# Optimization experiments

Hardware: AMD Instinct MI355X
Metric: run time of the kernel (lower is better)

The kernel has to match this reference:

```python
import jax, jax.numpy as jnp
import numpy as np

N = 50000        # nodes
E = 800000       # edges (before self-loops)
F_IN = 128       # input_features
HID = 160        # hidden_sf(5) * model_dim(32)
OUT_C = 128      # out_sf(4) * output_channels(32)
NGR = 64         # number of graphs in batch
OUT_DIM = 10
K = 5            # hops per SGConv


def setup_inputs() -> dict:
    key = jax.random.key(0)
    ks = jax.random.split(key, 12)
    x = jax.random.normal(ks[0], (N, F_IN), dtype=jnp.float32)
    edge_index = jax.random.randint(ks[1], (2, E), 0, N, dtype=jnp.int64)
    batch = jnp.sort(jax.random.randint(ks[2], (N,), 0, NGR, dtype=jnp.int64))
    s = 0.05
    W1 = jax.random.normal(ks[3], (F_IN, HID), dtype=jnp.float32) * s
    b1 = jnp.zeros((HID,), dtype=jnp.float32)
    W2 = jax.random.normal(ks[4], (HID, HID), dtype=jnp.float32) * s
    b2 = jnp.zeros((HID,), dtype=jnp.float32)
    W3 = jax.random.normal(ks[5], (HID, OUT_C), dtype=jnp.float32) * s
    b3 = jnp.zeros((OUT_C,), dtype=jnp.float32)
    fc_w = jax.random.normal(ks[6], (OUT_C, OUT_DIM), dtype=jnp.float32) * s
    fc_b = jnp.zeros((OUT_DIM,), dtype=jnp.float32)
    return {"x": x, "edge_index": edge_index, "batch": batch,
            "W1": W1, "b1": b1, "W2": W2, "b2": b2, "W3": W3, "b3": b3,
            "fc_w": fc_w, "fc_b": fc_b}


def reference(x, edge_index, batch, W1, b1, W2, b2, W3, b3, fc_w, fc_b):
    # gcn_norm: add self-loops, symmetric normalization D^-1/2 A D^-1/2
    loop = jnp.arange(N, dtype=edge_index.dtype)
    src = jnp.concatenate([edge_index[0], loop])   # [E+N]
    dst = jnp.concatenate([edge_index[1], loop])
    deg = jax.ops.segment_sum(jnp.ones(E + N, dtype=x.dtype), dst, num_segments=N)
    dinv = jnp.where(deg > 0, deg ** -0.5, 0.0)
    norm = (dinv[src] * dinv[dst])[:, None]        # [E+N, 1]

    def prop(h):
        # one hop of normalized propagation: gather at src, scatter-add at dst
        return jax.ops.segment_sum(h[src] * norm, dst, num_segments=N)

    def sgconv(h, W, b):
        for _ in range(K):
            h = prop(h)
        return h @ W + b

    h = sgconv(x, W1, b1)
    h = sgconv(h, W2, b2)
    h = sgconv(h, W3, b3)

    # global_mean_pool over batch indices
    counts = jax.ops.segment_sum(jnp.ones(N, dtype=h.dtype), batch, num_segments=NGR)
    pooled = jax.ops.segment_sum(h, batch, num_segments=NGR)
    pooled = pooled / jnp.maximum(counts, 1.0)[:, None]

    logits = pooled @ fc_w + fc_b
    return jax.nn.log_softmax(logits, axis=1)
```

## Files before the change

### kernel.cpp

```cpp
#include <hip/hip_runtime.h>

constexpr int N    = 50000;
constexpr int E    = 800000;
constexpr int NG   = 64;
constexpr int ODIM = 10;
constexpr int OUTC = 128;
constexpr int GP_BLOCKS = 256;
constexpr int SCAN_B = (N + 255) / 256;
constexpr int CS1B   = 784;
constexpr float SCALE    = 32768.0f;
constexpr float INVSCALE = 1.0f / SCALE;

constexpr int CNT_C = 16;
constexpr int CHUNK = E / CNT_C;
constexpr int CNT_R = 8;
constexpr int RANGE = N / CNT_R;
constexpr int NV4   = CHUNK / 4;
constexpr int HV4   = NV4 / 2;

typedef float floatx2 __attribute__((ext_vector_type(2)));

__device__ __forceinline__ void unp4(unsigned int u, float* f) {
    floatx2 lo = __builtin_amdgcn_cvt_pk_f32_fp8(u, false);
    floatx2 hi = __builtin_amdgcn_cvt_pk_f32_fp8(u, true);
    f[0] = lo.x; f[1] = lo.y; f[2] = hi.x; f[3] = hi.y;
}
__device__ __forceinline__ unsigned int pk4(float a, float b, float c, float d) {
    int r = __builtin_amdgcn_cvt_pk_fp8_f32(a, b, 0, false);
    r = __builtin_amdgcn_cvt_pk_fp8_f32(c, d, r, true);
    return (unsigned int)r;
}

__global__ void k_init_small(int* cntg, float* svec) {
    int i = threadIdx.x;
    if (i < NG) cntg[i] = 0;
    if (i < 128) svec[i] = 0.f;
}

__device__ __forceinline__ void cnt4_src(int4 v, int lo, int* h,
                                         int* __restrict__ pos_e, int e) {
    if ((unsigned)(v.x - lo) < (unsigned)RANGE) pos_e[e]     = atomicAdd(&h[v.x - lo], 1);
    if ((unsigned)(v.y - lo) < (unsigned)RANGE) pos_e[e + 1] = atomicAdd(&h[v.y - lo], 1);
    if ((unsigned)(v.z - lo) < (unsigned)RANGE) pos_e[e + 2] = atomicAdd(&h[v.z - lo], 1);
    if ((unsigned)(v.w - lo) < (unsigned)RANGE) pos_e[e + 3] = atomicAdd(&h[v.w - lo], 1);
}
__device__ __forceinline__ void cnt4_dst(int4 v, int lo, int* h) {
    if ((unsigned)(v.x - lo) < (unsigned)RANGE) atomicAdd(&h[v.x - lo], 1);
    if ((unsigned)(v.y - lo) < (unsigned)RANGE) atomicAdd(&h[v.y - lo], 1);
    if ((unsigned)(v.z - lo) < (unsigned)RANGE) atomicAdd(&h[v.z - lo], 1);
    if ((unsigned)(v.w - lo) < (unsigned)RANGE) atomicAdd(&h[v.w - lo], 1);
}

__global__ __launch_bounds__(512) void k_count(const int* __restrict__ ei,
        int* __restrict__ cnt16, int* __restrict__ deg16, int* __restrict__ pos_e) {
    __shared__ int h[RANGE];
    int bid  = blockIdx.x;
    int c    = bid & 15;
    int r    = (bid >> 4) & 7;
    int kind = bid >> 7;
    int tid  = threadIdx.x;
    for (int i = tid; i < RANGE; i += 512) h[i] = 0;
    __syncthreads();
    int lo = r * RANGE;
    const int4* src = (const int4*)(ei + (size_t)kind * E + (size_t)c * CHUNK);
    int ebase = c * CHUNK;
    if (kind == 0) {
        for (int i = tid; i < HV4; i += 512) {
            int4 a = src[i];
            int4 b = src[i + HV4];
            cnt4_src(a, lo, h, pos_e, ebase + i * 4);
            cnt4_src(b, lo, h, pos_e, ebase + (i + HV4) * 4);
        }
    } else {
        for (int i = tid; i < HV4; i += 512) {
            int4 a = src[i];
            int4 b = src[i + HV4];
            cnt4_dst(a, lo, h);
            cnt4_dst(b, lo, h);
        }
    }
    __syncthreads();
    int* dst = (kind == 0 ? cnt16 : deg16) + (size_t)c * N + lo;
    for (int i = tid; i < RANGE; i += 512) dst[i] = h[i];
}

__global__ void k_scan1(const int* __restrict__ cnt16, int* __restrict__ base16,
                        int* __restrict__ off, int* bsum,
                        const int* __restrict__ deg16, float* wsq, float* sdeg) {
    __shared__ int buf[256];
    int tid = threadIdx.x;
    int i = blockIdx.x * 256 + tid;
    int total = 0;
    if (i < N) {
        int run = 0;
        #pragma unroll
        for (int q = 0; q < CNT_C; ++q) {
            base16[q * N + i] = run;
            run += cnt16[q * N + i];
        }
        total = run;
        int deg = 1;
        #pragma unroll
        for (int q = 0; q < CNT_C; ++q) deg += deg16[q * N + i];
        float d = (float)deg;
        wsq[i]  = 1.0f / d;
        sdeg[i] = sqrtf(d);
    }
    buf[tid] = total;
    __syncthreads();
    for (int s = 1; s < 256; s <<= 1) {
        int add = (tid >= s) ? buf[tid - s] : 0;
        __syncthreads();
        buf[tid] += add;
        __syncthreads();
    }
    if (i < N) off[i] = buf[tid] - total;
    if (tid == 255) bsum[blockIdx.x] = buf[255];
}

__global__ void k_scan2(int* bsum, int* off) {
    __shared__ int buf[256];
    int tid = threadIdx.x;
    int v = (tid < SCAN_B) ? bsum[tid] : 0;
    buf[tid] = v;
    __syncthreads();
    for (int s = 1; s < 256; s <<= 1) {
        int add = (tid >= s) ? buf[tid - s] : 0;
        __syncthreads();
        buf[tid] += add;
        __syncthreads();
    }
    if (tid < SCAN_B) bsum[tid] = buf[tid] - v;
    if (tid == 0) off[N] = E;
}

__global__ void k_scan3(int* off, const int* __restrict__ bsum) {
    int i = blockIdx.x * 256 + threadIdx.x;
    if (i < N) off[i] += bsum[blockIdx.x];
}

__global__ void k_cntg(const int* __restrict__ batch, int* cntg) {
    __shared__ int h[NG];
    if (threadIdx.x < NG) h[threadIdx.x] = 0;
    __syncthreads();
    int i = blockIdx.x * 256 + threadIdx.x;
    if (i < N) atomicAdd(&h[batch[i]], 1);
    __syncthreads();
    if (threadIdx.x < NG && h[threadIdx.x]) atomicAdd(&cntg[threadIdx.x], h[threadIdx.x]);
}

__global__ void k_fill(const int* __restrict__ ei, const int* __restrict__ off,
                       const int* __restrict__ base16, const int* __restrict__ pos_e,
                       int* __restrict__ mdst,
                       const int* __restrict__ batch, const int* __restrict__ cntg,
                       const float* __restrict__ sdeg, uint4* Z0) {
    int e = blockIdx.x * 256 + threadIdx.x;
    if (e < E) {
        int s = ei[e];
        int q = e / CHUNK;
        mdst[off[s] + base16[q * N + s] + pos_e[e]] = ei[E + e];
    }
    if (e < N) {
        int i = e;
        int g = batch[i];
        int c = cntg[g]; if (c < 1) c = 1;
        float v = (SCALE / (float)c) / sdeg[i];
        unsigned int byte = (unsigned int)(__builtin_amdgcn_cvt_pk_fp8_f32(v, v, 0, false) & 0xFF);
        uint4 rows[4];
        #pragma unroll
        for (int q = 0; q < 4; ++q) rows[q] = make_uint4(0u, 0u, 0u, 0u);
        unsigned int* wp = (unsigned int*)rows;
        wp[g >> 2] = byte << (8 * (g & 3));
        #pragma unroll
        for (int q = 0; q < 4; ++q) Z0[(size_t)i * 4 + q] = rows[q];
    }
}

__device__ __forceinline__ void add16(float* acc, uint4 g) {
    float f[16];
    unp4(g.x, f); unp4(g.y, f + 4); unp4(g.z, f + 8); unp4(g.w, f + 12);
    #pragma unroll
    for (int k = 0; k < 16; ++k) acc[k] += f[k];
}

__global__ __launch_bounds__(256) void k_prop(
        const uint4* __restrict__ zin, uint2* __restrict__ zout,
        const int* __restrict__ off, const int* __restrict__ mdst,
        const float* __restrict__ wsq) {
    int t = blockIdx.x * 256 + threadIdx.x;
    int node = t >> 3;
    int sub  = (t >> 2) & 1;
    int c    = t & 3;
    if (node >= N) return;

    float acc[16];
    #pragma unroll
    for (int k = 0; k < 16; ++k) acc[k] = 0.f;

    int a = off[node], b = off[node + 1];
    int half = (b - a + 1) >> 1;
    int e  = sub ? a + half : a;
    int e1 = sub ? b : a + half;
    if (!sub) {
        add16(acc, zin[(size_t)node * 4 + c]);
    }
    for (; e + 7 < e1; e += 8) {
        int d0 = mdst[e],     d1 = mdst[e + 1], d2 = mdst[e + 2], d3 = mdst[e + 3];
        int d4 = mdst[e + 4], d5 = mdst[e + 5], d6 = mdst[e + 6], d7 = mdst[e + 7];
        uint4 g0 = zin[(size_t)d0 * 4 + c];
        uint4 g1 = zin[(size_t)d1 * 4 + c];
        uint4 g2 = zin[(size_t)d2 * 4 + c];
        uint4 g3 = zin[(size_t)d3 * 4 + c];
        uint4 g4 = zin[(size_t)d4 * 4 + c];
        uint4 g5 = zin[(size_t)d5 * 4 + c];
        uint4 g6 = zin[(size_t)d6 * 4 + c];
        uint4 g7 = zin[(size_t)d7 * 4 + c];
        add16(acc, g0); add16(acc, g1); add16(acc, g2); add16(acc, g3);
        add16(acc, g4); add16(acc, g5); add16(acc, g6); add16(acc, g7);
    }
    for (; e + 3 < e1; e += 4) {
        int d0 = mdst[e], d1 = mdst[e + 1], d2 = mdst[e + 2], d3 = mdst[e + 3];
        uint4 g0 = zin[(size_t)d0 * 4 + c];
        uint4 g1 = zin[(size_t)d1 * 4 + c];
        uint4 g2 = zin[(size_t)d2 * 4 + c];
        uint4 g3 = zin[(size_t)d3 * 4 + c];
        add16(acc, g0); add16(acc, g1); add16(acc, g2); add16(acc, g3);
    }
    for (; e < e1; ++e) {
        add16(acc, zin[(size_t)mdst[e] * 4 + c]);
    }

    #pragma unroll
    for (int k = 0; k < 16; ++k) acc[k] += __shfl_xor(acc[k], 4, 64);

    float ws = wsq[node];
    uint2 o;
    if (sub == 0) {
        o.x = pk4(ws * acc[0],  ws * acc[1],  ws * acc[2],  ws * acc[3]);
        o.y = pk4(ws * acc[4],  ws * acc[5],  ws * acc[6],  ws * acc[7]);
    } else {
        o.x = pk4(ws * acc[8],  ws * acc[9],  ws * acc[10], ws * acc[11]);
        o.y = pk4(ws * acc[12], ws * acc[13], ws * acc[14], ws * acc[15]);
    }
    zout[(size_t)node * 8 + c * 2 + sub] = o;
}

__global__ void k_colsum1(const unsigned int* __restrict__ Z,
                          const float* __restrict__ sdeg, float* __restrict__ part2) {
    __shared__ float red[256];
    int g = threadIdx.x & 63, sub = threadIdx.x >> 6;
    int w = g >> 2;
    int word = (g >> 1) & 1;
    int odd  = g & 1;
    float acc = 0.f;
    for (int i = blockIdx.x * 4 + sub; i < N; i += gridDim.x * 4) {
        unsigned int u = Z[(size_t)i * 16 + w];
        floatx2 p = word ? __builtin_amdgcn_cvt_pk_f32_fp8(u, true)
                         : __builtin_amdgcn_cvt_pk_f32_fp8(u, false);
        acc += (odd ? p.y : p.x) * sdeg[i];
    }
    red[threadIdx.x] = acc;
    __syncthreads();
    if (sub == 0)
        part2[g * CS1B + blockIdx.x] = red[g] + red[64 + g] + red[128 + g] + red[192 + g];
}

__global__ void k_colsum2(const float* __restrict__ part2, float* __restrict__ sdst) {
    __shared__ float red[256];
    int g = blockIdx.x, tid = threadIdx.x;
    float acc = 0.f;
    for (int b = tid; b < CS1B; b += 256) acc += part2[g * CS1B + b];
    red[tid] = acc;
    __syncthreads();
    for (int s = 128; s >= 1; s >>= 1) {
        if (tid < s) red[tid] += red[tid + s];
        __syncthreads();
    }
    if (tid == 0) sdst[g] = red[0] * INVSCALE;
}

__global__ __launch_bounds__(256) void k_gpart(
        const uint4* __restrict__ Z, const float4* __restrict__ X,
        const float* __restrict__ sdeg, float* part) {
    __shared__ unsigned int zr[32][16];
    __shared__ float xr[32][128];
    __shared__ float sd[32];
    int tid = threadIdx.x;
    int f4 = tid & 31;
    int gs = tid >> 5;
    float4 acc[8];
    #pragma unroll
    for (int k = 0; k < 8; ++k) acc[k] = make_float4(0.f, 0.f, 0.f, 0.f);

    int per = (N + gridDim.x - 1) / gridDim.x;
    int n0 = blockIdx.x * per;
    int n1 = n0 + per; if (n1 > N) n1 = N;

    for (int nb = n0; nb < n1; nb += 32) {
        __syncthreads();
        if (tid < 128) {
            int nn = tid >> 2, q = tid & 3;
            int node = nb + nn;
            uint4 zv = make_uint4(0u, 0u, 0u, 0u);
            if (node < n1) zv = Z[(size_t)node * 4 + q];
            ((uint4*)&zr[nn][0])[q] = zv;
        }
        if (tid >= 192 && tid < 224) {
            int node = nb + (tid - 192);
            sd[tid - 192] = (node < n1) ? sdeg[node] : 0.f;
        }
        #pragma unroll
        for (int r = 0; r < 4; ++r) {
            int l = r * 256 + tid;
            int nn = l >> 5, c4 = l & 31;
            int node = nb + nn;
            float4 xv = make_float4(0.f, 0.f, 0.f, 0.f);
            if (node < n1) xv = X[(size_t)node * 32 + c4];
            ((float4*)&xr[nn][0])[c4] = xv;
        }
        __syncthreads();
        for (int nn = 0; nn < 32; ++nn) {
            float sc = sd[nn];
            float4 xv = ((const float4*)&xr[nn][0])[f4];
            xv.x *= sc; xv.y *= sc; xv.z *= sc; xv.w *= sc;
            unsigned int za = zr[nn][gs * 2], zb = zr[nn][gs * 2 + 1];
            float zf[8];
            unp4(za, zf); unp4(zb, zf + 4);
            #pragma unroll
            for (int k = 0; k < 8; ++k) {
                acc[k].x += zf[k] * xv.x; acc[k].y += zf[k] * xv.y;
                acc[k].z += zf[k] * xv.z; acc[k].w += zf[k] * xv.w;
            }
        }
    }
    float4* dst = (float4*)(part + (size_t)blockIdx.x * 8192);
    #pragma unroll
    for (int k = 0; k < 8; ++k) dst[(gs * 8 + k) * 32 + f4] = acc[k];
}

__global__ void k_greduce(const float4* __restrict__ part, float4* G) {
    __shared__ float4 red[256];
    int tid = threadIdx.x;
    int o4 = blockIdx.x * 16 + (tid & 15);
    int slice = tid >> 4;
    float4 a = make_float4(0.f, 0.f, 0.f, 0.f);
    #pragma unroll 4
    for (int k = 0; k < GP_BLOCKS / 16; ++k) {
        float4 v = part[(size_t)(slice * (GP_BLOCKS / 16) + k) * 2048 + o4];
        a.x += v.x; a.y += v.y; a.z += v.z; a.w += v.w;
    }
    red[tid] = a;
    __syncthreads();
    for (int s = 128; s >= 16; s >>= 1) {
        if (tid < s) {
            float4 b = red[tid + s];
            red[tid].x += b.x; red[tid].y += b.y; red[tid].z += b.z; red[tid].w += b.w;
        }
        __syncthreads();
    }
    if (tid < 16) {
        float4 r = red[tid];
        G[o4] = make_float4(r.x * INVSCALE, r.y * INVSCALE, r.z * INVSCALE, r.w * INVSCALE);
    }
}

__global__ void k_pass1(const float* __restrict__ W1, const float* __restrict__ b1,
                        const float* __restrict__ W2, float* T1c) {
    int t = blockIdx.x * 256 + threadIdx.x;
    if (t >= 129 * 160) return;
    int m = t / 160, c = t - m * 160;
    const float* arow = (m < 128) ? (W1 + m * 160) : b1;
    float a = 0.f;
    for (int k = 0; k < 160; ++k) a += arow[k] * W2[k * 160 + c];
    T1c[t] = a;
}

__global__ void k_pass2(const float* __restrict__ T1c, const float* __restrict__ b2,
                        const float* __restrict__ W3, float* TWc) {
    int t = blockIdx.x * 256 + threadIdx.x;
    if (t >= 130 * 128) return;
    int m = t >> 7, c = t & 127;
    const float* arow = (m < 129) ? (T1c + m * 160) : b2;
    float a = 0.f;
    for (int k = 0; k < 160; ++k) a += arow[k] * W3[k * 128 + c];
    TWc[t] = a;
}

__global__ void k_pooled(const float* __restrict__ G, const float* __restrict__ TWc,
                         const float* __restrict__ b3, const float* __restrict__ svec,
                         float* pooled) {
    int t = blockIdx.x * 256 + threadIdx.x;
    if (t >= NG * OUTC) return;
    int g = t >> 7, f = t & 127;
    float a = b3[f] + svec[64 + g] * TWc[128 * 128 + f] + svec[g] * TWc[129 * 128 + f];
    for (int k = 0; k < 128; ++k) a += G[g * 128 + k] * TWc[k * 128 + f];
    pooled[t] = a;
}

__global__ void k_head(const float* __restrict__ pooled, const float* __restrict__ fcw,
                       const float* __restrict__ fcb, float* out) {
    __shared__ float lg[ODIM];
    int g = blockIdx.x, tid = threadIdx.x;
    if (tid < ODIM) {
        float a = fcb[tid];
        for (int k = 0; k < 128; ++k) a += pooled[g * 128 + k] * fcw[k * ODIM + tid];
        lg[tid] = a;
    }
    __syncthreads();
    if (tid == 0) {
        float mx = lg[0];
        for (int j = 1; j < ODIM; ++j) mx = fmaxf(mx, lg[j]);
        float sum = 0.f;
        for (int j = 0; j < ODIM; ++j) sum += expf(lg[j] - mx);
        float lse = mx + logf(sum);
        for (int j = 0; j < ODIM; ++j) out[g * ODIM + j] = lg[j] - lse;
    }
}

extern "C" void kernel_launch(void* const* d_in, const int* in_sizes, int n_in,
                              void* d_out, int out_size, void* d_ws, size_t ws_size,
                              hipStream_t stream) {
    const float* x    = (const float*)d_in[0];
    const int*   ei   = (const int*)d_in[1];
    const int*   batch= (const int*)d_in[2];
    const float* W1   = (const float*)d_in[3];
    const float* b1   = (const float*)d_in[4];
    const float* W2   = (const float*)d_in[5];
    const float* b2   = (const float*)d_in[6];
    const float* W3   = (const float*)d_in[7];
    const float* b3   = (const float*)d_in[8];
    const float* fcw  = (const float*)d_in[9];
    const float* fcb  = (const float*)d_in[10];
    float* out = (float*)d_out;

    char* p = (char*)d_ws;
    auto alloc = [&](size_t bytes) -> void* {
        void* r = (void*)p;
        p += (bytes + 255) & ~(size_t)255;
        return r;
    };
    int*   cnt16   = (int*)  alloc((size_t)CNT_C * N * 4);
    int*   deg16   = (int*)  alloc((size_t)CNT_C * N * 4);
    int*   base16  = (int*)  alloc((size_t)CNT_C * N * 4);
    float* wsq     = (float*)alloc((size_t)N * 4);
    float* sdeg    = (float*)alloc((size_t)N * 4);
    int*   off     = (int*)  alloc((size_t)(N + 1) * 4);
    int*   bsum    = (int*)  alloc((size_t)SCAN_B * 4);
    int*   pos_e   = (int*)  alloc((size_t)E * 4);
    int*   mdst    = (int*)  alloc((size_t)E * 4);
    int*   cntg    = (int*)  alloc((size_t)NG * 4);
    float* svec    = (float*)alloc(128 * 4);
    unsigned char* Z0 = (unsigned char*)alloc((size_t)N * 64);
    unsigned char* Z1 = (unsigned char*)alloc((size_t)N * 64);
    float* part    = (float*)alloc((size_t)GP_BLOCKS * 8192 * 4);
    float* G       = (float*)alloc(8192 * 4);
    float* T1c     = (float*)alloc(129 * 160 * 4);
    float* TWc     = (float*)alloc(130 * 128 * 4);
    float* pooled  = (float*)alloc(64 * 128 * 4);

    int nb_n = (N + 255) / 256;
    int nb_e = (E + 255) / 256;
    k_init_small<<<1, 256, 0, stream>>>(cntg, svec);
    k_count<<<CNT_C * CNT_R * 2, 512, 0, stream>>>(ei, cnt16, deg16, pos_e);
    k_scan1<<<SCAN_B, 256, 0, stream>>>(cnt16, base16, off, bsum, deg16, wsq, sdeg);
    k_scan2<<<1, 256, 0, stream>>>(bsum, off);
    k_scan3<<<SCAN_B, 256, 0, stream>>>(off, bsum);
    k_cntg<<<nb_n, 256, 0, stream>>>(batch, cntg);
    k_fill<<<nb_e, 256, 0, stream>>>(ei, off, base16, pos_e, mdst, batch, cntg, sdeg, (uint4*)Z0);

    unsigned char* zc = Z0;
    unsigned char* zn = Z1;
    for (int hop = 1; hop <= 15; ++hop) {
        k_prop<<<(N * 8 + 255) / 256, 256, 0, stream>>>(
            (const uint4*)zc, (uint2*)zn, off, mdst, wsq);
        unsigned char* t = zc; zc = zn; zn = t;
        if (hop == 5) {
            k_colsum1<<<CS1B, 256, 0, stream>>>((const unsigned int*)zc, sdeg, part);
            k_colsum2<<<64, 256, 0, stream>>>(part, svec);
        }
        if (hop == 10) {
            k_colsum1<<<CS1B, 256, 0, stream>>>((const unsigned int*)zc, sdeg, part);
            k_colsum2<<<64, 256, 0, stream>>>(part, svec + 64);
        }
    }

    k_gpart<<<GP_BLOCKS, 256, 0, stream>>>((const uint4*)zc, (const float4*)x, sdeg, part);
    k_greduce<<<128, 256, 0, stream>>>((const float4*)part, (float4*)G);

    k_pass1<<<(129 * 160 + 255) / 256, 256, 0, stream>>>(W1, b1, W2, T1c);
    k_pass2<<<(130 * 128 + 255) / 256, 256, 0, stream>>>(T1c, b2, W3, TWc);
    k_pooled<<<32, 256, 0, stream>>>(G, TWc, b3, svec, pooled);
    k_head<<<NG, 64, 0, stream>>>(pooled, fcw, fcb, out);
}
```

Measured before the change: 448.7 us.

## Use one 4-thread group per node in propagation with deeper gather unroll

The propagation kernel previously split each node's edge list between two 4-thread halves and merged the halves with a cross-lane shuffle. Now each node is handled by a single 4-thread group that walks all of its edges and writes one 16-byte output per thread, which halves the thread count and removes the shuffle. The gather loop adds a 16-wide unrolled stage, edge indices are loaded with nontemporal hints, and launch bounds request 3 blocks per CU. The trade-off is less parallelism per node and more registers from the wider unroll, with fewer threads available to hide gather latency.

Measured after the change: 671.9 us. 49.7% more time.

```diff
diff --git a/kernel.cpp b/kernel.cpp
--- a/kernel.cpp
+++ b/kernel.cpp
@@ -183,13 +183,12 @@
     for (int k = 0; k < 16; ++k) acc[k] += f[k];
 }
 
-__global__ __launch_bounds__(256) void k_prop(
-        const uint4* __restrict__ zin, uint2* __restrict__ zout,
+__global__ __launch_bounds__(256, 3) void k_prop(
+        const uint4* __restrict__ zin, uint4* __restrict__ zout,
         const int* __restrict__ off, const int* __restrict__ mdst,
         const float* __restrict__ wsq) {
     int t = blockIdx.x * 256 + threadIdx.x;
-    int node = t >> 3;
-    int sub  = (t >> 2) & 1;
+    int node = t >> 2;
     int c    = t & 3;
     if (node >= N) return;
 
@@ -197,52 +196,51 @@
     #pragma unroll
     for (int k = 0; k < 16; ++k) acc[k] = 0.f;
 
-    int a = off[node], b = off[node + 1];
-    int half = (b - a + 1) >> 1;
-    int e  = sub ? a + half : a;
-    int e1 = sub ? b : a + half;
-    if (!sub) {
-        add16(acc, zin[(size_t)node * 4 + c]);
+    int e  = off[node];
+    int e1 = off[node + 1];
+    add16(acc, zin[(size_t)node * 4 + c]);
+
+    for (; e + 15 < e1; e += 16) {
+        int d[16];
+        #pragma unroll
+        for (int j = 0; j < 16; ++j) d[j] = __builtin_nontemporal_load(mdst + e + j);
+        uint4 g[16];
+        #pragma unroll
+        for (int j = 0; j < 16; ++j) g[j] = zin[(size_t)d[j] * 4 + c];
+        #pragma unroll
+        for (int j = 0; j < 16; ++j) add16(acc, g[j]);
     }
     for (; e + 7 < e1; e += 8) {
-        int d0 = mdst[e],     d1 = mdst[e + 1], d2 = mdst[e + 2], d3 = mdst[e + 3];
-        int d4 = mdst[e + 4], d5 = mdst[e + 5], d6 = mdst[e + 6], d7 = mdst[e + 7];
-        uint4 g0 = zin[(size_t)d0 * 4 + c];
-        uint4 g1 = zin[(size_t)d1 * 4 + c];
-        uint4 g2 = zin[(size_t)d2 * 4 + c];
-        uint4 g3 = zin[(size_t)d3 * 4 + c];
-        uint4 g4 = zin[(size_t)d4 * 4 + c];
-        uint4 g5 = zin[(size_t)d5 * 4 + c];
-        uint4 g6 = zin[(size_t)d6 * 4 + c];
-        uint4 g7 = zin[(size_t)d7 * 4 + c];
-        add16(acc, g0); add16(acc, g1); add16(acc, g2); add16(acc, g3);
-        add16(acc, g4); add16(acc, g5); add16(acc, g6); add16(acc, g7);
+        int d[8];
+        #pragma unroll
+        for (int j = 0; j < 8; ++j) d[j] = __builtin_nontemporal_load(mdst + e + j);
+        uint4 g[8];
+        #pragma unroll
+        for (int j = 0; j < 8; ++j) g[j] = zin[(size_t)d[j] * 4 + c];
+        #pragma unroll
+        for (int j = 0; j < 8; ++j) add16(acc, g[j]);
     }
     for (; e + 3 < e1; e += 4) {
-        int d0 = mdst[e], d1 = mdst[e + 1], d2 = mdst[e + 2], d3 = mdst[e + 3];
-        uint4 g0 = zin[(size_t)d0 * 4 + c];
-        uint4 g1 = zin[(size_t)d1 * 4 + c];
-        uint4 g2 = zin[(size_t)d2 * 4 + c];
-        uint4 g3 = zin[(size_t)d3 * 4 + c];
-        add16(acc, g0); add16(acc, g1); add16(acc, g2); add16(acc, g3);
+        int d[4];
+        #pragma unroll
+        for (int j = 0; j < 4; ++j) d[j] = __builtin_nontemporal_load(mdst + e + j);
+        uint4 g[4];
+        #pragma unroll
+        for (int j = 0; j < 4; ++j) g[j] = zin[(size_t)d[j] * 4 + c];
+        #pragma unroll
+        for (int j = 0; j < 4; ++j) add16(acc, g[j]);
     }
     for (; e < e1; ++e) {
-        add16(acc, zin[(size_t)mdst[e] * 4 + c]);
-    }
-
-    #pragma unroll
-    for (int k = 0; k < 16; ++k) acc[k] += __shfl_xor(acc[k], 4, 64);
+        add16(acc, zin[(size_t)__builtin_nontemporal_load(mdst + e) * 4 + c]);
+    }
 
     float ws = wsq[node];
-    uint2 o;
-    if (sub == 0) {
-        o.x = pk4(ws * acc[0],  ws * acc[1],  ws * acc[2],  ws * acc[3]);
-        o.y = pk4(ws * acc[4],  ws * acc[5],  ws * acc[6],  ws * acc[7]);
-    } else {
-        o.x = pk4(ws * acc[8],  ws * acc[9],  ws * acc[10], ws * acc[11]);
-        o.y = pk4(ws * acc[12], ws * acc[13], ws * acc[14], ws * acc[15]);
-    }
-    zout[(size_t)node * 8 + c * 2 + sub] = o;
+    uint4 o;
+    o.x = pk4(ws * acc[0],  ws * acc[1],  ws * acc[2],  ws * acc[3]);
+    o.y = pk4(ws * acc[4],  ws * acc[5],  ws * acc[6],  ws * acc[7]);
+    o.z = pk4(ws * acc[8],  ws * acc[9],  ws * acc[10], ws * acc[11]);
+    o.w = pk4(ws * acc[12], ws * acc[13], ws * acc[14], ws * acc[15]);
+    zout[(size_t)node * 4 + c] = o;
 }
 
 __global__ void k_colsum1(const unsigned int* __restrict__ Z,
@@ -471,8 +469,8 @@
     unsigned char* zc = Z0;
     unsigned char* zn = Z1;
     for (int hop = 1; hop <= 15; ++hop) {
-        k_prop<<<(N * 8 + 255) / 256, 256, 0, stream>>>(
-            (const uint4*)zc, (uint2*)zn, off, mdst, wsq);
+        k_prop<<<(N * 4 + 255) / 256, 256, 0, stream>>>(
+            (const uint4*)zc, (uint4*)zn, off, mdst, wsq);
         unsigned char* t = zc; zc = zn; zn = t;
         if (hop == 5) {
             k_colsum1<<<CS1B, 256, 0, stream>>>((const unsigned int*)zc, sdeg, part);
```
